# Performance work log

Hardware: AMD Instinct MI355X
Metric: run time of the kernel (lower is better)

Reference implementation:

```python
import jax, jax.numpy as jnp
import numpy as np

T = 512        # sequence / max_length
I = 512        # input_dim
H = 1024       # hidden_size
O = 1          # output_size
L = 512        # max_length (attention logits)


def setup_inputs() -> dict:
    key = jax.random.key(0)
    ks = jax.random.split(key, 14)
    s = 0.02
    return {
        "input_seq": jax.random.normal(ks[0], (T, I), jnp.float32),
        "target_seq": jax.random.normal(ks[1], (T, O), jnp.float32),
        # encoder LSTM (input I -> hidden H), PyTorch gate order i,f,g,o
        "W_ih_e": jax.random.normal(ks[2], (4 * H, I), jnp.float32) * s,
        "W_hh_e": jax.random.normal(ks[3], (4 * H, H), jnp.float32) * s,
        "b_ih_e": jnp.zeros((4 * H,), jnp.float32),
        "b_hh_e": jnp.zeros((4 * H,), jnp.float32),
        # attention: Linear(2H -> L)
        "W_attn": jax.random.normal(ks[4], (L, 2 * H), jnp.float32) * s,
        "b_attn": jnp.zeros((L,), jnp.float32),
        # decoder LSTM (input 2H -> hidden H)
        "W_ih_d": jax.random.normal(ks[5], (4 * H, 2 * H), jnp.float32) * s,
        "W_hh_d": jax.random.normal(ks[6], (4 * H, H), jnp.float32) * s,
        "b_ih_d": jnp.zeros((4 * H,), jnp.float32),
        "b_hh_d": jnp.zeros((4 * H,), jnp.float32),
        # output Linear(H -> O)
        "W_out": jax.random.normal(ks[7], (O, H), jnp.float32) * s,
        "b_out": jnp.zeros((O,), jnp.float32),
    }


def _lstm_cell(x, h, c, Wih, Whh, bih, bhh):
    gates = Wih @ x + bih + Whh @ h + bhh          # [4H]
    i, f, g, o = jnp.split(gates, 4)
    c = jax.nn.sigmoid(f) * c + jax.nn.sigmoid(i) * jnp.tanh(g)
    h = jax.nn.sigmoid(o) * jnp.tanh(c)
    return h, c


def reference(input_seq, target_seq, W_ih_e, W_hh_e, b_ih_e, b_hh_e,
              W_attn, b_attn, W_ih_d, W_hh_d, b_ih_d, b_hh_d, W_out, b_out):
    Th = input_seq.shape[0]
    max_len = W_attn.shape[0]
    hid = W_hh_e.shape[1]

    def step(carry, xs):
        eh, ec, dh, dc, aw = carry
        x_t, i = xs
        eh, ec = _lstm_cell(x_t, eh, ec, W_ih_e, W_hh_e, b_ih_e, b_hh_e)
        energy = W_attn @ jnp.concatenate([eh, dh]) + b_attn   # [L]
        aw = aw.at[i].set(energy[i])
        aw = jax.nn.softmax(aw)                                 # re-softmaxed each step, as in source
        context = aw[i] * eh                                    # [H]
        din = jnp.concatenate([context, dh])                    # [2H]
        dh, dc = _lstm_cell(din, dh, dc, W_ih_d, W_hh_d, b_ih_d, b_hh_d)
        out_t = W_out @ dh + b_out                              # [O]
        return (eh, ec, dh, dc, aw), out_t

    z = jnp.zeros((hid,), input_seq.dtype)
    carry0 = (z, z, z, z, jnp.zeros((max_len,), input_seq.dtype))
    _, output_seq = jax.lax.scan(step, carry0, (input_seq, jnp.arange(Th)))
    return output_seq  # [T, O]
```

## Files before the change

kernel.cpp:

```cpp
#include <hip/hip_runtime.h>
#include <math.h>


#define T_STEPS 512
#define ENC_BLK 128
#define NBLK    256
#define NTHR    512
#define POLL_LIMIT 30000u

typedef float fv4 __attribute__((ext_vector_type(4)));

__device__ __forceinline__ float sigf(float x) { return 1.0f / (1.0f + expf(-x)); }

__device__ __forceinline__ float ld_f(const float* p) {
  return __hip_atomic_load(p, __ATOMIC_RELAXED, __HIP_MEMORY_SCOPE_AGENT);
}

__device__ __forceinline__ void st_bypass4(float* p, float v) {
  asm volatile("global_store_dword %0, %1, off sc0 sc1"
               :: "v"(p), "v"(v) : "memory");
}

__device__ __forceinline__ bool valid4(fv4 v) {
  return __float_as_uint(v.x) != 0xAAAAAAAAu && __float_as_uint(v.y) != 0xAAAAAAAAu &&
         __float_as_uint(v.z) != 0xAAAAAAAAu && __float_as_uint(v.w) != 0xAAAAAAAAu;
}
__device__ __forceinline__ bool validf(float a, float b, float c, float d) {
  return __float_as_uint(a) != 0xAAAAAAAAu && __float_as_uint(b) != 0xAAAAAAAAu &&
         __float_as_uint(c) != 0xAAAAAAAAu && __float_as_uint(d) != 0xAAAAAAAAu;
}

template <int SLP>
__device__ __forceinline__ fv4 poll2(const float* p, int* okp) {
  fv4 a, b;
  int ok = 1;
  asm volatile("global_load_dwordx4 %0, %1, off sc0 sc1" : "=v"(a) : "v"(p) : "memory");
  for (unsigned it = 0;; ++it) {
    asm volatile("global_load_dwordx4 %0, %1, off sc0 sc1" : "=v"(b) : "v"(p) : "memory");
    asm volatile("s_waitcnt vmcnt(1)" : "+v"(a) :: "memory");
    if (valid4(a)) { asm volatile("s_waitcnt vmcnt(0)" ::: "memory"); break; }
    asm volatile("global_load_dwordx4 %0, %1, off sc0 sc1" : "=v"(a) : "v"(p) : "memory");
    asm volatile("s_waitcnt vmcnt(1)" : "+v"(b) :: "memory");
    if (valid4(b)) { asm volatile("s_waitcnt vmcnt(0)" ::: "memory"); a = b; break; }
    if (it > POLL_LIMIT) { ok = 0; asm volatile("s_waitcnt vmcnt(0)" ::: "memory"); break; }
    if (SLP) __builtin_amdgcn_s_sleep(SLP);
  }
  *okp = ok;
  return a;
}

__device__ __forceinline__ fv4 ld_once4(const float* p) {
  fv4 a;
  asm volatile("global_load_dwordx4 %0, %1, off sc0 sc1" : "=v"(a) : "v"(p) : "memory");
  asm volatile("s_waitcnt vmcnt(0)" : "+v"(a) :: "memory");
  return a;
}

__global__ __launch_bounds__(256) void prep_gemm(const float* __restrict__ X,
                                                 const float* __restrict__ Wih,
                                                 const float* __restrict__ bih,
                                                 const float* __restrict__ bhh,
                                                 float* __restrict__ px) {
  __shared__ float Ws[64][68];
  __shared__ float Xs[64][68];
  const int r0 = blockIdx.x * 64;
  const int t0 = blockIdx.y * 64;
  const int tid = threadIdx.x;
  const int tr = tid & 15;
  const int tc = tid >> 4;
  float acc[4][4] = {{0.f}};
  for (int k0 = 0; k0 < 512; k0 += 64) {
    __syncthreads();
    const int lr = tid >> 4;
    const int lc = (tid & 15) * 4;
#pragma unroll
    for (int rep = 0; rep < 4; rep++) {
      const int row = lr + rep * 16;
      const float4 wv = *(const float4*)&Wih[(size_t)(r0 + row) * 512 + k0 + lc];
      Ws[lc + 0][row] = wv.x; Ws[lc + 1][row] = wv.y;
      Ws[lc + 2][row] = wv.z; Ws[lc + 3][row] = wv.w;
      const float4 xv = *(const float4*)&X[(size_t)(t0 + row) * 512 + k0 + lc];
      Xs[row][lc + 0] = xv.x; Xs[row][lc + 1] = xv.y;
      Xs[row][lc + 2] = xv.z; Xs[row][lc + 3] = xv.w;
    }
    __syncthreads();
    for (int kk = 0; kk < 64; kk++) {
      float a[4], x[4];
#pragma unroll
      for (int i = 0; i < 4; i++) a[i] = Ws[kk][tr * 4 + i];
#pragma unroll
      for (int j = 0; j < 4; j++) x[j] = Xs[tc * 4 + j][kk];
#pragma unroll
      for (int i = 0; i < 4; i++)
#pragma unroll
        for (int j = 0; j < 4; j++) acc[i][j] += a[i] * x[j];
    }
  }
#pragma unroll
  for (int i = 0; i < 4; i++) {
    const int r = r0 + tr * 4 + i;
    const int g = r >> 10, h = r & 1023;
    const float bsum = bih[r] + bhh[r];
#pragma unroll
    for (int j = 0; j < 4; j++) {
      const int t = t0 + tc * 4 + j;
      px[((size_t)t * 1024 + h) * 4 + g] = acc[i][j] + bsum;
    }
  }
}

__global__ __launch_bounds__(512, 1) void lstm_persist(
    const float* __restrict__ Whhe, const float* __restrict__ Wattn,
    const float* __restrict__ battn, const float* __restrict__ Wihd,
    const float* __restrict__ Whhd, const float* __restrict__ bihd,
    const float* __restrict__ bhhd, const float* __restrict__ Wout,
    const float* __restrict__ bout, const float* __restrict__ px,
    float* ehbuf, float* dhbuf, float* out) {
  __shared__ float4 xbuf[256];
  __shared__ float4 dbuf[256];
  __shared__ float  aw[512];
  __shared__ float  GA[32];
  __shared__ float  GB[32];
  __shared__ float  bd[32];
  __shared__ float  redE[4];
  __shared__ float  redE2[4];
  __shared__ float  red[8];
  __shared__ float  red2[4];
  __shared__ int    sbad;

  const int b    = blockIdx.x;
  const int tid  = threadIdx.x;
  const int w    = tid >> 6;
  const int lane = tid & 63;
  const int ri   = lane & 3;
  const int s16  = lane >> 2;
  const int g    = w >> 1;
  const int j    = ((w & 1) << 2) + ri;

  if (b < ENC_BLK) {
    const int e = b;
    const int r = (g << 10) + (e << 3) + j;
    float4 we[16];
#pragma unroll
    for (int k = 0; k < 16; k++) {
      const int m = (k + s16) & 15;
      we[k] = *(const float4*)&Whhe[(size_t)r * 1024 + s16 * 64 + m * 4];
    }
    if (tid < 256) xbuf[tid] = make_float4(0.f, 0.f, 0.f, 0.f);
    if (tid == 0) sbad = 0;
    float ec = 0.f;
    __syncthreads();

    for (int t = 0; t < T_STEPS; t++) {
      float ge = 0.f;
#pragma unroll
      for (int k = 0; k < 16; k++) {
        const int m = (k + s16) & 15;
        const float4 x = xbuf[s16 * 16 + m];
        ge += we[k].x * x.x + we[k].y * x.y + we[k].z * x.z + we[k].w * x.w;
      }
      if (s16 == 0) ge += px[((size_t)t * 1024 + (e << 3) + j) * 4 + g];
      ge += __shfl_xor(ge, 4, 64);
      ge += __shfl_xor(ge, 8, 64);
      ge += __shfl_xor(ge, 16, 64);
      ge += __shfl_xor(ge, 32, 64);
      if (lane < 4) GA[w * 4 + lane] = ge;
      __syncthreads();
      if (tid < 8) {
        const float gi = GA[tid], gf = GA[8 + tid], gg = GA[16 + tid], go = GA[24 + tid];
        const float c = sigf(gf) * ec + sigf(gi) * tanhf(gg);
        ec = c;
        const float h = sigf(go) * tanhf(c);
        st_bypass4(&ehbuf[(size_t)t * 1024 + (e << 3) + tid], h);
      }
      if (tid >= 256 && tid < 272) {
        int oks;
        const int sg = ((e << 1) + ((tid - 256) << 4)) & 255;
        (void)poll2<0>(&ehbuf[(size_t)t * 1024 + sg * 4], &oks);
      }
      __syncthreads();
      int ok = 1;
      if (tid < 256) {
        fv4 ev = ld_once4(&ehbuf[(size_t)t * 1024 + tid * 4]);
        if (!valid4(ev)) ev = poll2<0>(&ehbuf[(size_t)t * 1024 + tid * 4], &ok);
        xbuf[tid] = make_float4(ev.x, ev.y, ev.z, ev.w);
      }
      if (!ok) sbad = 1;
      __syncthreads();
      if (sbad) break;
    }
  } else {
    const int d = b - ENC_BLK;
    const int r = (g << 10) + (d << 3) + j;
    float4 w1[16], wr[16];
#pragma unroll
    for (int k = 0; k < 16; k++) {
      const int m = (k + s16) & 15;
      w1[k] = *(const float4*)&Wihd[(size_t)r * 2048 + s16 * 64 + m * 4];
      const float4 a = *(const float4*)&Wihd[(size_t)r * 2048 + 1024 + s16 * 64 + m * 4];
      const float4 c = *(const float4*)&Whhd[(size_t)r * 1024 + s16 * 64 + m * 4];
      wr[k] = make_float4(a.x + c.x, a.y + c.y, a.z + c.z, a.w + c.w);
    }
    if (tid < 32) {
      const int gg2 = tid >> 3, jj2 = tid & 7;
      bd[tid] = bihd[(gg2 << 10) + (d << 3) + jj2] + bhhd[(gg2 << 10) + (d << 3) + jj2];
    }
    aw[tid] = 0.f;
    if (tid < 256) {
      xbuf[tid] = make_float4(0.f, 0.f, 0.f, 0.f);
      dbuf[tid] = make_float4(0.f, 0.f, 0.f, 0.f);
    }
    if (tid == 0) sbad = 0;
    float dc = 0.f;
    float4 wo = make_float4(0.f, 0.f, 0.f, 0.f);
    if (tid < 256) wo = *(const float4*)&Wout[tid * 4];
    const float boutv = bout[0];
    __syncthreads();

    float es0 = 0.f, es1 = 0.f, es2 = 0.f, es3 = 0.f;
    if (tid < 256) {
      const float* pe = &ehbuf[(size_t)tid * 4];
      es0 = ld_f(pe + 0); es1 = ld_f(pe + 1); es2 = ld_f(pe + 2); es3 = ld_f(pe + 3);
    }

    bool failed = false;
    for (int t = 0; t < T_STEPS; t++) {
      const float battn_t = battn[t];
      const float ex0 = expf(aw[tid]);
      float so = (tid == t) ? 0.f : ex0;
#pragma unroll
      for (int mk = 1; mk <= 32; mk <<= 1) so += __shfl_xor(so, mk, 64);
      if (lane == 0) red[w] = so;

      float4 wae = make_float4(0.f, 0.f, 0.f, 0.f);
      float4 wad = make_float4(0.f, 0.f, 0.f, 0.f);
      float epe = 0.f;
      int ok1 = 1;
      if (tid < 256) {
        wae = *(const float4*)&Wattn[(size_t)t * 2048 + tid * 4];
        wad = *(const float4*)&Wattn[(size_t)t * 2048 + 1024 + tid * 4];
        fv4 ev;
        if (validf(es0, es1, es2, es3)) {
          ev.x = es0; ev.y = es1; ev.z = es2; ev.w = es3;
        } else {
          ev = poll2<8>(&ehbuf[(size_t)t * 1024 + tid * 4], &ok1);
        }
        epe = wae.x * ev.x + wae.y * ev.y + wae.z * ev.z + wae.w * ev.w;
        xbuf[tid] = make_float4(ev.x, ev.y, ev.z, ev.w);
      }
      if (!ok1) sbad = 1;
#pragma unroll
      for (int mk = 1; mk <= 32; mk <<= 1) epe += __shfl_xor(epe, mk, 64);
      if (lane == 0 && w < 4) redE[w] = epe;
      __syncthreads();
      if (sbad) { failed = true; break; }

      float ds0 = 0.f, ds1 = 0.f, ds2 = 0.f, ds3 = 0.f;
      if (t > 0 && tid < 256) {
        const float* pd = &dhbuf[(size_t)(t - 1) * 1024 + tid * 4];
        ds0 = ld_f(pd + 0); ds1 = ld_f(pd + 1); ds2 = ld_f(pd + 2); ds3 = ld_f(pd + 3);
      }

      float g1 = 0.f;
#pragma unroll
      for (int k = 0; k < 16; k++) {
        const int m = (k + s16) & 15;
        const float4 x = xbuf[s16 * 16 + m];
        g1 += w1[k].x * x.x + w1[k].y * x.y + w1[k].z * x.z + w1[k].w * x.w;
      }
      g1 += __shfl_xor(g1, 4, 64);
      g1 += __shfl_xor(g1, 8, 64);
      g1 += __shfl_xor(g1, 16, 64);
      g1 += __shfl_xor(g1, 32, 64);
      if (lane < 4) GA[w * 4 + lane] = g1;

      float epd = 0.f;
      int ok2 = 1;
      if (t > 0 && tid < 256) {
        fv4 dv;
        if (validf(ds0, ds1, ds2, ds3)) {
          dv.x = ds0; dv.y = ds1; dv.z = ds2; dv.w = ds3;
        } else {
          dv = poll2<4>(&dhbuf[(size_t)(t - 1) * 1024 + tid * 4], &ok2);
        }
        epd = wad.x * dv.x + wad.y * dv.y + wad.z * dv.z + wad.w * dv.w;
        dbuf[tid] = make_float4(dv.x, dv.y, dv.z, dv.w);
      }
      if (!ok2) sbad = 1;
#pragma unroll
      for (int mk = 1; mk <= 32; mk <<= 1) epd += __shfl_xor(epd, mk, 64);
      if (lane == 0 && w < 4) redE2[w] = epd;
      __syncthreads();
      if (sbad) { failed = true; break; }

      float g2 = 0.f;
#pragma unroll
      for (int k = 0; k < 16; k++) {
        const int m = (k + s16) & 15;
        const float4 dd = dbuf[s16 * 16 + m];
        g2 += wr[k].x * dd.x + wr[k].y * dd.y + wr[k].z * dd.z + wr[k].w * dd.w;
      }
      g2 += __shfl_xor(g2, 4, 64);
      g2 += __shfl_xor(g2, 8, 64);
      g2 += __shfl_xor(g2, 16, 64);
      g2 += __shfl_xor(g2, 32, 64);
      if (lane < 4) GB[w * 4 + lane] = g2;

      const float e_t = redE[0] + redE[1] + redE[2] + redE[3] +
                        redE2[0] + redE2[1] + redE2[2] + redE2[3] + battn_t;
      const float exden = expf(e_t);
      const float inv = 1.f / (red[0] + red[1] + red[2] + red[3] +
                               red[4] + red[5] + red[6] + red[7] + exden);
      const float awt = exden * inv;
      aw[tid] = ((tid == t) ? exden : ex0) * inv;
      __syncthreads();

      if (tid < 8) {
        const float gi = awt * GA[tid]      + GB[tid]      + bd[tid];
        const float gf = awt * GA[8 + tid]  + GB[8 + tid]  + bd[8 + tid];
        const float gg = awt * GA[16 + tid] + GB[16 + tid] + bd[16 + tid];
        const float go = awt * GA[24 + tid] + GB[24 + tid] + bd[24 + tid];
        const float c = sigf(gf) * dc + sigf(gi) * tanhf(gg);
        dc = c;
        const float h = sigf(go) * tanhf(c);
        st_bypass4(&dhbuf[(size_t)t * 1024 + (d << 3) + tid], h);
      }

      if (tid < 256) {
        const int tn = (t + 1 < T_STEPS) ? (t + 1) : t;
        const float* pe = &ehbuf[(size_t)tn * 1024 + tid * 4];
        es0 = ld_f(pe + 0); es1 = ld_f(pe + 1); es2 = ld_f(pe + 2); es3 = ld_f(pe + 3);
      }
    }

    if (!failed) {
#pragma unroll
      for (int i = 0; i < 4; i++) {
        const int t = d * 4 + i;
        float op = 0.f;
        int ok = 1;
        if (tid < 256) {
          const fv4 dv = poll2<0>(&dhbuf[(size_t)t * 1024 + tid * 4], &ok);
          op = wo.x * dv.x + wo.y * dv.y + wo.z * dv.z + wo.w * dv.w;
        }
        if (!ok) break;
#pragma unroll
        for (int mk = 1; mk <= 32; mk <<= 1) op += __shfl_xor(op, mk, 64);
        if (lane == 0 && w < 4) red2[w] = op;
        __syncthreads();
        if (tid == 0) out[t] = red2[0] + red2[1] + red2[2] + red2[3] + boutv;
        __syncthreads();
      }
    }
  }
}

extern "C" void kernel_launch(void* const* d_in, const int* in_sizes, int n_in,
                              void* d_out, int out_size, void* d_ws, size_t ws_size,
                              hipStream_t stream) {
  const float* X     = (const float*)d_in[0];
  const float* Wihe  = (const float*)d_in[2];
  const float* Whhe  = (const float*)d_in[3];
  const float* bihe  = (const float*)d_in[4];
  const float* bhhe  = (const float*)d_in[5];
  const float* Wattn = (const float*)d_in[6];
  const float* battn = (const float*)d_in[7];
  const float* Wihd  = (const float*)d_in[8];
  const float* Whhd  = (const float*)d_in[9];
  const float* bihd  = (const float*)d_in[10];
  const float* bhhd  = (const float*)d_in[11];
  const float* Wo    = (const float*)d_in[12];
  const float* bo    = (const float*)d_in[13];
  float* out = (float*)d_out;

  float* ws    = (float*)d_ws;
  float* px    = ws;
  float* ehbuf = px + (size_t)T_STEPS * 1024 * 4;
  float* dhbuf = ehbuf + (size_t)T_STEPS * 1024;
  const size_t need = ((size_t)T_STEPS * 1024 * 6) * sizeof(float);
  if (ws_size < need) return;

  prep_gemm<<<dim3(64, 8), 256, 0, stream>>>(X, Wihe, bihe, bhhe, px);
  lstm_persist<<<NBLK, NTHR, 0, stream>>>(
      Whhe, Wattn, battn, Wihd, Whhd, bihd, bhhd, Wo, bo, px, ehbuf, dhbuf, out);
}
```

Measured before the change: 1.773 ms.

## Replace sentinel data polling with atomic counter flags for cross-block step sync

Encoder and decoder blocks now increment striped per-step atomic counters after writing their hidden-state slice and spin on four counters before reading the step's data. This replaces many threads polling 0xAAAA sentinel values in the hidden buffers. The sleep in the decoder's poll loops is removed, and readers block-wide agree (syncthreads_and) before falling back to a flag wait. The aim is lower polling traffic and latency per recurrent step. In exchange it adds atomic contention on four counters, a memset launch, and a relaxed-ordering dependence on the vmcnt wait before the bump.

```diff
diff --git a/kernel.cpp b/kernel.cpp
--- a/kernel.cpp
+++ b/kernel.cpp
@@ -7,6 +7,7 @@
 #define NBLK    256
 #define NTHR    512
 #define POLL_LIMIT 30000u
+#define FLAG_LIMIT 20000u
 
 typedef float fv4 __attribute__((ext_vector_type(4)));
 
@@ -30,7 +31,6 @@
          __float_as_uint(c) != 0xAAAAAAAAu && __float_as_uint(d) != 0xAAAAAAAAu;
 }
 
-template <int SLP>
 __device__ __forceinline__ fv4 poll2(const float* p, int* okp) {
   fv4 a, b;
   int ok = 1;
@@ -43,7 +43,6 @@
     asm volatile("s_waitcnt vmcnt(1)" : "+v"(b) :: "memory");
     if (valid4(b)) { asm volatile("s_waitcnt vmcnt(0)" ::: "memory"); a = b; break; }
     if (it > POLL_LIMIT) { ok = 0; asm volatile("s_waitcnt vmcnt(0)" ::: "memory"); break; }
-    if (SLP) __builtin_amdgcn_s_sleep(SLP);
   }
   *okp = ok;
   return a;
@@ -54,6 +53,22 @@
   asm volatile("global_load_dwordx4 %0, %1, off sc0 sc1" : "=v"(a) : "v"(p) : "memory");
   asm volatile("s_waitcnt vmcnt(0)" : "+v"(a) :: "memory");
   return a;
+}
+
+__device__ __forceinline__ void flag_bump(unsigned* f) {
+  asm volatile("s_waitcnt vmcnt(0)" ::: "memory");
+  __hip_atomic_fetch_add(f, 1u, __ATOMIC_RELAXED, __HIP_MEMORY_SCOPE_AGENT);
+}
+
+__device__ __forceinline__ int flag_wait(const unsigned* f, unsigned tgt) {
+  for (unsigned it = 0;; ++it) {
+    const unsigned a = __hip_atomic_load(f +  0, __ATOMIC_RELAXED, __HIP_MEMORY_SCOPE_AGENT);
+    const unsigned b = __hip_atomic_load(f + 32, __ATOMIC_RELAXED, __HIP_MEMORY_SCOPE_AGENT);
+    const unsigned c = __hip_atomic_load(f + 64, __ATOMIC_RELAXED, __HIP_MEMORY_SCOPE_AGENT);
+    const unsigned d = __hip_atomic_load(f + 96, __ATOMIC_RELAXED, __HIP_MEMORY_SCOPE_AGENT);
+    if (a >= tgt && b >= tgt && c >= tgt && d >= tgt) return 1;
+    if (it > FLAG_LIMIT) return 0;
+  }
 }
 
 __global__ __launch_bounds__(256) void prep_gemm(const float* __restrict__ X,
@@ -115,7 +130,7 @@
     const float* __restrict__ Whhd, const float* __restrict__ bihd,
     const float* __restrict__ bhhd, const float* __restrict__ Wout,
     const float* __restrict__ bout, const float* __restrict__ px,
-    float* ehbuf, float* dhbuf, float* out) {
+    float* ehbuf, float* dhbuf, unsigned* flags, float* out) {
   __shared__ float4 xbuf[256];
   __shared__ float4 dbuf[256];
   __shared__ float  aw[512];
@@ -128,6 +143,9 @@
   __shared__ float  red2[4];
   __shared__ int    sbad;
 
+  unsigned* flagsE = flags;
+  unsigned* flagsD = flags + 128;
+
   const int b    = blockIdx.x;
   const int tid  = threadIdx.x;
   const int w    = tid >> 6;
@@ -149,6 +167,7 @@
     if (tid < 256) xbuf[tid] = make_float4(0.f, 0.f, 0.f, 0.f);
     if (tid == 0) sbad = 0;
     float ec = 0.f;
+    int fE_alive = 1;
     __syncthreads();
 
     for (int t = 0; t < T_STEPS; t++) {
@@ -173,16 +192,15 @@
         const float h = sigf(go) * tanhf(c);
         st_bypass4(&ehbuf[(size_t)t * 1024 + (e << 3) + tid], h);
       }
-      if (tid >= 256 && tid < 272) {
-        int oks;
-        const int sg = ((e << 1) + ((tid - 256) << 4)) & 255;
-        (void)poll2<0>(&ehbuf[(size_t)t * 1024 + sg * 4], &oks);
+      if (tid == 0) {
+        flag_bump(&flagsE[(e & 3) * 32]);
+        if (fE_alive) fE_alive = flag_wait(flagsE, 32u * (t + 1));
       }
       __syncthreads();
       int ok = 1;
       if (tid < 256) {
         fv4 ev = ld_once4(&ehbuf[(size_t)t * 1024 + tid * 4]);
-        if (!valid4(ev)) ev = poll2<0>(&ehbuf[(size_t)t * 1024 + tid * 4], &ok);
+        if (!valid4(ev)) ev = poll2(&ehbuf[(size_t)t * 1024 + tid * 4], &ok);
         xbuf[tid] = make_float4(ev.x, ev.y, ev.z, ev.w);
       }
       if (!ok) sbad = 1;
@@ -212,6 +230,7 @@
     }
     if (tid == 0) sbad = 0;
     float dc = 0.f;
+    int fE_alive = 1, fD_alive = 1;
     float4 wo = make_float4(0.f, 0.f, 0.f, 0.f);
     if (tid < 256) wo = *(const float4*)&Wout[tid * 4];
     const float boutv = bout[0];
@@ -234,16 +253,26 @@
 
       float4 wae = make_float4(0.f, 0.f, 0.f, 0.f);
       float4 wad = make_float4(0.f, 0.f, 0.f, 0.f);
+      int myok = 1;
+      if (tid < 256) {
+        wae = *(const float4*)&Wattn[(size_t)t * 2048 + tid * 4];
+        wad = *(const float4*)&Wattn[(size_t)t * 2048 + 1024 + tid * 4];
+        myok = validf(es0, es1, es2, es3);
+      }
+      const int allok = __syncthreads_and(myok);
+      if (!allok) {
+        if (tid == 0 && fE_alive) fE_alive = flag_wait(flagsE, 32u * (t + 1));
+        __syncthreads();
+      }
       float epe = 0.f;
       int ok1 = 1;
       if (tid < 256) {
-        wae = *(const float4*)&Wattn[(size_t)t * 2048 + tid * 4];
-        wad = *(const float4*)&Wattn[(size_t)t * 2048 + 1024 + tid * 4];
         fv4 ev;
-        if (validf(es0, es1, es2, es3)) {
+        if (allok) {
           ev.x = es0; ev.y = es1; ev.z = es2; ev.w = es3;
         } else {
-          ev = poll2<8>(&ehbuf[(size_t)t * 1024 + tid * 4], &ok1);
+          ev = ld_once4(&ehbuf[(size_t)t * 1024 + tid * 4]);
+          if (!valid4(ev)) ev = poll2(&ehbuf[(size_t)t * 1024 + tid * 4], &ok1);
         }
         epe = wae.x * ev.x + wae.y * ev.y + wae.z * ev.z + wae.w * ev.w;
         xbuf[tid] = make_float4(ev.x, ev.y, ev.z, ev.w);
@@ -273,6 +302,9 @@
       g1 += __shfl_xor(g1, 16, 64);
       g1 += __shfl_xor(g1, 32, 64);
       if (lane < 4) GA[w * 4 + lane] = g1;
+
+      if (t > 0 && tid == 0 && fD_alive) fD_alive = flag_wait(flagsD, 32u * t);
+      __syncthreads();
 
       float epd = 0.f;
       int ok2 = 1;
@@ -281,7 +313,8 @@
         if (validf(ds0, ds1, ds2, ds3)) {
           dv.x = ds0; dv.y = ds1; dv.z = ds2; dv.w = ds3;
         } else {
-          dv = poll2<4>(&dhbuf[(size_t)(t - 1) * 1024 + tid * 4], &ok2);
+          dv = ld_once4(&dhbuf[(size_t)(t - 1) * 1024 + tid * 4]);
+          if (!valid4(dv)) dv = poll2(&dhbuf[(size_t)(t - 1) * 1024 + tid * 4], &ok2);
         }
         epd = wad.x * dv.x + wad.y * dv.y + wad.z * dv.z + wad.w * dv.w;
         dbuf[tid] = make_float4(dv.x, dv.y, dv.z, dv.w);
@@ -325,6 +358,7 @@
         const float h = sigf(go) * tanhf(c);
         st_bypass4(&dhbuf[(size_t)t * 1024 + (d << 3) + tid], h);
       }
+      if (tid == 0) flag_bump(&flagsD[(d & 3) * 32]);
 
       if (tid < 256) {
         const int tn = (t + 1 < T_STEPS) ? (t + 1) : t;
@@ -340,7 +374,7 @@
         float op = 0.f;
         int ok = 1;
         if (tid < 256) {
-          const fv4 dv = poll2<0>(&dhbuf[(size_t)t * 1024 + tid * 4], &ok);
+          const fv4 dv = poll2(&dhbuf[(size_t)t * 1024 + tid * 4], &ok);
           op = wo.x * dv.x + wo.y * dv.y + wo.z * dv.z + wo.w * dv.w;
         }
         if (!ok) break;
@@ -377,10 +411,13 @@
   float* px    = ws;
   float* ehbuf = px + (size_t)T_STEPS * 1024 * 4;
   float* dhbuf = ehbuf + (size_t)T_STEPS * 1024;
-  const size_t need = ((size_t)T_STEPS * 1024 * 6) * sizeof(float);
+  unsigned* flags = (unsigned*)(dhbuf + (size_t)T_STEPS * 1024);
+  const size_t need = ((size_t)T_STEPS * 1024 * 6) * sizeof(float) + 1024;
   if (ws_size < need) return;
 
+  hipMemsetAsync(flags, 0, 1024, stream);
   prep_gemm<<<dim3(64, 8), 256, 0, stream>>>(X, Wihe, bihe, bhhe, px);
   lstm_persist<<<NBLK, NTHR, 0, stream>>>(
-      Whhe, Wattn, battn, Wihd, Whhd, bihd, bhhd, Wo, bo, px, ehbuf, dhbuf, out);
-}
+      Whhe, Wattn, battn, Wihd, Whhd, bihd, bhhd, Wo, bo, px, ehbuf, dhbuf,
+      flags, out);
+}
```

New measurement: 2.130 ms. 20.1% more time.
